# Kernel tuning notes

Hardware: AMD Instinct MI355X
Metric: run time of the kernel (lower is better)

The kernel has to match this reference:

```python
import jax, jax.numpy as jnp
import numpy as np

NH = 16  # n_heads

def setup_inputs() -> dict:
    key = jax.random.key(0)
    ks = jax.random.split(key, 5)
    B, T, D = 2, 2048, 2048
    scale = 0.02
    return {
        "x": jax.random.normal(ks[0], (B, T, D), dtype=jnp.float32),
        "Wq": jax.random.normal(ks[1], (D, D), dtype=jnp.float32) * scale,
        "Wk": jax.random.normal(ks[2], (D, D), dtype=jnp.float32) * scale,
        "Wv": jax.random.normal(ks[3], (D, D), dtype=jnp.float32) * scale,
        "Wo": jax.random.normal(ks[4], (D, D), dtype=jnp.float32) * scale,
    }

def reference(x, Wq, Wk, Wv, Wo):
    B, T, D = x.shape
    hd = D // NH
    # torch nn.Linear(d,d,bias=False): y = x @ W.T
    q = (x @ Wq.T).reshape(B, T, NH, hd).transpose(0, 2, 1, 3)  # [B,H,T,hd]
    k = (x @ Wk.T).reshape(B, T, NH, hd).transpose(0, 2, 1, 3)
    v = (x @ Wv.T).reshape(B, T, NH, hd).transpose(0, 2, 1, 3)
    att = jnp.einsum('bhtd,bhsd->bhts', q, k) / jnp.sqrt(jnp.asarray(hd, x.dtype))
    neg = jnp.finfo(att.dtype).min
    mask = jnp.triu(jnp.full((T, T), neg, dtype=att.dtype), k=1)  # causal
    att = att + mask
    w = jax.nn.softmax(att, axis=-1)
    z = jnp.einsum('bhts,bhsd->bhtd', w, v)  # [B,H,T,hd]
    z = z.transpose(0, 2, 1, 3).reshape(B, T, D)
    return z @ Wo.T
```

## Files before the change

kernel.cpp:

```cpp
#include <hip/hip_runtime.h>
#include <hip/hip_bf16.h>
#include <math.h>


typedef __attribute__((ext_vector_type(4))) float  f32x4;
typedef __attribute__((ext_vector_type(8))) __bf16 bf16x8;

union Pack8 { __bf16 h[8]; uint4 u; };
union Pack4 { __bf16 h[4]; uint2 u; };

__device__ __forceinline__ void async16(const void* g, void* l) {
    __builtin_amdgcn_global_load_lds((const __attribute__((address_space(1))) void*)g,
                                     (__attribute__((address_space(3))) void*)l, 16, 0, 0);
}

struct CvtArgs { const float* s[5]; __bf16* d[5]; };

__global__ __launch_bounds__(256) void cvt_all(CvtArgs a) {
    int i = blockIdx.x * 256 + threadIdx.x;
    int t, off;
    if (i < (1 << 20)) { t = 0; off = i; }
    else { int j = i - (1 << 20); t = 1 + (j >> 19); off = j & ((1 << 19) - 1); }
    const float4* s = (const float4*)a.s[t] + (size_t)off * 2;
    float4 f0 = s[0], f1 = s[1];
    Pack8 pk;
    pk.h[0] = (__bf16)f0.x; pk.h[1] = (__bf16)f0.y;
    pk.h[2] = (__bf16)f0.z; pk.h[3] = (__bf16)f0.w;
    pk.h[4] = (__bf16)f1.x; pk.h[5] = (__bf16)f1.y;
    pk.h[6] = (__bf16)f1.z; pk.h[7] = (__bf16)f1.w;
    ((uint4*)a.d[t])[off] = pk.u;
}

__global__ __launch_bounds__(256) void gemm_qkv(const __bf16* __restrict__ A,
        const __bf16* __restrict__ Wq, const __bf16* __restrict__ Wk,
        const __bf16* __restrict__ Wv,
        __bf16* __restrict__ Qo, __bf16* __restrict__ Ko, __bf16* __restrict__ Vt) {
    constexpr int K = 2048, N = 2048, MT = 4096;
    __shared__ __bf16 lds[32 * 512];
    __bf16* Af = lds;
    __bf16* Bf = lds + 16 * 512;
    const int tid  = threadIdx.x;
    const int w    = tid >> 6;
    const int lane = tid & 63;
    const int lm   = lane & 15;
    const int quad = lane >> 4;
    const int seg  = blockIdx.x >> 4;
    const int col0 = (blockIdx.x & 15) * 128;
    const int row0 = blockIdx.y * 128;
    const __bf16* B = (seg == 0) ? Wq : (seg == 1) ? Wk : Wv;
    const int mw = (w >> 1) * 4;
    const int nw = (w & 1) * 4;

    const __bf16* gp = (w < 2)
        ? A + (size_t)(row0 + (w * 4) * 16 + lm) * K + quad * 8
        : B + (size_t)(col0 + ((w - 2) * 4) * 16 + lm) * K + quad * 8;
    __bf16* ldst = (w < 2) ? Af + (w * 8) * 512 : Bf + ((w - 2) * 8) * 512;

    f32x4 acc[4][4] = {};

    for (int k0 = 0; k0 < K; k0 += 64) {
        __syncthreads();
#pragma unroll
        for (int i = 0; i < 8; ++i)
            async16(gp + k0 + (i >> 1) * (16 * K) + (i & 1) * 32, ldst + i * 512);
        __syncthreads();

#pragma unroll
        for (int kh = 0; kh < 2; ++kh) {
            bf16x8 af[4], bfv[4];
#pragma unroll
            for (int mt = 0; mt < 4; ++mt)
                af[mt] = *(const bf16x8*)(Af + ((mw + mt) * 2 + kh) * 512 + lane * 8);
#pragma unroll
            for (int nt = 0; nt < 4; ++nt)
                bfv[nt] = *(const bf16x8*)(Bf + ((nw + nt) * 2 + kh) * 512 + lane * 8);
#pragma unroll
            for (int mt = 0; mt < 4; ++mt)
#pragma unroll
                for (int nt = 0; nt < 4; ++nt)
                    acc[mt][nt] = __builtin_amdgcn_mfma_f32_16x16x32_bf16(
                        af[mt], bfv[nt], acc[mt][nt], 0, 0, 0);
        }
    }

    if (seg < 2) {
        __bf16* C = seg ? Ko : Qo;
#pragma unroll
        for (int mt = 0; mt < 4; ++mt)
#pragma unroll
            for (int nt = 0; nt < 4; ++nt)
#pragma unroll
                for (int r = 0; r < 4; ++r)
                    C[(size_t)(row0 + (mw + mt) * 16 + quad * 4 + r) * N +
                      col0 + (nw + nt) * 16 + lm] = (__bf16)acc[mt][nt][r];
    } else {
#pragma unroll
        for (int mt = 0; mt < 4; ++mt)
#pragma unroll
            for (int nt = 0; nt < 4; ++nt) {
                Pack4 p;
#pragma unroll
                for (int r = 0; r < 4; ++r) p.h[r] = (__bf16)acc[mt][nt][r];
                *(uint2*)&Vt[(size_t)(col0 + (nw + nt) * 16 + lm) * MT +
                             row0 + (mw + mt) * 16 + quad * 4] = p.u;
            }
    }
}

__global__ __launch_bounds__(256) void gemm_wo(const __bf16* __restrict__ A,
                                               const __bf16* __restrict__ B,
                                               float* __restrict__ C) {
    constexpr int K = 2048, N = 2048;
    __shared__ __bf16 lds[32 * 512];
    __bf16* Af = lds;
    __bf16* Bf = lds + 16 * 512;
    const int tid  = threadIdx.x;
    const int w    = tid >> 6;
    const int lane = tid & 63;
    const int lm   = lane & 15;
    const int quad = lane >> 4;
    const int row0 = blockIdx.y * 128;
    const int col0 = blockIdx.x * 128;
    const int mw   = (w >> 1) * 4;
    const int nw   = (w & 1) * 4;

    const __bf16* gp = (w < 2)
        ? A + (size_t)(row0 + (w * 4) * 16 + lm) * K + quad * 8
        : B + (size_t)(col0 + ((w - 2) * 4) * 16 + lm) * K + quad * 8;
    __bf16* ldst = (w < 2) ? Af + (w * 8) * 512 : Bf + ((w - 2) * 8) * 512;

    f32x4 acc[4][4] = {};

    for (int k0 = 0; k0 < K; k0 += 64) {
        __syncthreads();
#pragma unroll
        for (int i = 0; i < 8; ++i)
            async16(gp + k0 + (i >> 1) * (16 * K) + (i & 1) * 32, ldst + i * 512);
        __syncthreads();

#pragma unroll
        for (int kh = 0; kh < 2; ++kh) {
            bf16x8 af[4], bfv[4];
#pragma unroll
            for (int mt = 0; mt < 4; ++mt)
                af[mt] = *(const bf16x8*)(Af + ((mw + mt) * 2 + kh) * 512 + lane * 8);
#pragma unroll
            for (int nt = 0; nt < 4; ++nt)
                bfv[nt] = *(const bf16x8*)(Bf + ((nw + nt) * 2 + kh) * 512 + lane * 8);
#pragma unroll
            for (int mt = 0; mt < 4; ++mt)
#pragma unroll
                for (int nt = 0; nt < 4; ++nt)
                    acc[mt][nt] = __builtin_amdgcn_mfma_f32_16x16x32_bf16(
                        af[mt], bfv[nt], acc[mt][nt], 0, 0, 0);
        }
    }

#pragma unroll
    for (int mt = 0; mt < 4; ++mt)
#pragma unroll
        for (int nt = 0; nt < 4; ++nt)
#pragma unroll
            for (int r = 0; r < 4; ++r)
                C[(size_t)(row0 + (mw + mt) * 16 + quad * 4 + r) * N +
                  col0 + (nw + nt) * 16 + lm] = acc[mt][nt][r];
}

__global__ __launch_bounds__(256) void attn5(const __bf16* __restrict__ Q,
                                             const __bf16* __restrict__ K,
                                             const __bf16* __restrict__ Vt,
                                             __bf16* __restrict__ Z) {
    constexpr int T = 2048, D = 2048, MT = 4096, PS = 72;
    __shared__ __bf16 Kf[16 * 512];
    __shared__ __bf16 Vf[16 * 512];
    __shared__ __bf16 Pf[4 * 16 * PS];
    const int tid  = threadIdx.x;
    const int w    = tid >> 6;
    const int lane = tid & 63;
    const int lm   = lane & 15;
    const int quad = lane >> 4;
    const int f    = blockIdx.x;
    const int bh   = ((f >> 7) << 3) | (f & 7);
    const int pair = (f >> 3) & 15;
    const int b    = bh >> 4;
    const int h    = bh & 15;

    const size_t qkbase = (size_t)b * T * D + (size_t)h * 128;
    const __bf16* Qh = Q + qkbase;
    const __bf16* Kh = K + qkbase;
    const __bf16* Vh = Vt + (size_t)(h * 128) * MT + (size_t)b * T;
    __bf16* Zh = Z + qkbase;

    bf16x8 ones;
#pragma unroll
    for (int i = 0; i < 8; ++i) ones[i] = (__bf16)1.0f;

    const float c = 0.08838834764831845f;
    __bf16* pw = Pf + w * (16 * PS);

    for (int ph = 0; ph < 2; ++ph) {
        const int j  = ph ? 31 - pair : pair;
        const int q0 = j * 64 + w * 16;

        bf16x8 qf[4];
#pragma unroll
        for (int kk = 0; kk < 4; ++kk)
            qf[kk] = *(const bf16x8*)(Qh + (size_t)(q0 + lm) * D + kk * 32 + quad * 8);

        f32x4 o[8] = {};
        f32x4 osum = {};

        for (int t = 0; t <= j; ++t) {
            const int kv0 = t * 64;
            __syncthreads();
#pragma unroll
            for (int i = 0; i < 4; ++i) {
                const int fk = w * 4 + i;
                const int nt = fk >> 2, kk = fk & 3;
                async16(Kh + (size_t)(kv0 + nt * 16 + lm) * D + kk * 32 + quad * 8,
                        Kf + fk * 512);
                const int on = fk >> 1, kc = fk & 1;
                async16(Vh + (size_t)(on * 16 + lm) * MT + kv0 + kc * 32 + quad * 8,
                        Vf + fk * 512);
            }
            __syncthreads();

            f32x4 s[4] = {};
#pragma unroll
            for (int nt = 0; nt < 4; ++nt)
#pragma unroll
                for (int kk = 0; kk < 4; ++kk) {
                    bf16x8 kfr = *(const bf16x8*)(Kf + (nt * 4 + kk) * 512 + lane * 8);
                    s[nt] = __builtin_amdgcn_mfma_f32_16x16x32_bf16(qf[kk], kfr, s[nt], 0, 0, 0);
                }

            const bool diag = (t == j);
#pragma unroll
            for (int nt = 0; nt < 4; ++nt)
#pragma unroll
                for (int r = 0; r < 4; ++r) {
                    float v = s[nt][r];
                    if (diag && (kv0 + nt * 16 + lm > q0 + quad * 4 + r)) v = -1e30f;
                    s[nt][r] = __expf(fmaf(v, c, -4.0f));
                }

#pragma unroll
            for (int nt = 0; nt < 4; ++nt)
#pragma unroll
                for (int r = 0; r < 4; ++r)
                    pw[(quad * 4 + r) * PS + nt * 16 + lm] = (__bf16)s[nt][r];

            bf16x8 pf[2];
#pragma unroll
            for (int kc = 0; kc < 2; ++kc)
                pf[kc] = *(const bf16x8*)(pw + lm * PS + kc * 32 + quad * 8);

#pragma unroll
            for (int kc = 0; kc < 2; ++kc) {
                osum = __builtin_amdgcn_mfma_f32_16x16x32_bf16(pf[kc], ones, osum, 0, 0, 0);
#pragma unroll
                for (int on = 0; on < 8; ++on) {
                    bf16x8 vf = *(const bf16x8*)(Vf + (on * 2 + kc) * 512 + lane * 8);
                    o[on] = __builtin_amdgcn_mfma_f32_16x16x32_bf16(pf[kc], vf, o[on], 0, 0, 0);
                }
            }
        }

        float inv[4];
#pragma unroll
        for (int r = 0; r < 4; ++r) inv[r] = 1.f / osum[r];
#pragma unroll
        for (int on = 0; on < 8; ++on)
#pragma unroll
            for (int r = 0; r < 4; ++r)
                Zh[(size_t)(q0 + quad * 4 + r) * D + on * 16 + lm] =
                    (__bf16)(o[on][r] * inv[r]);
    }
}

extern "C" void kernel_launch(void* const* d_in, const int* in_sizes, int n_in,
                              void* d_out, int out_size, void* d_ws, size_t ws_size,
                              hipStream_t stream) {
    const float* x  = (const float*)d_in[0];
    const float* Wq = (const float*)d_in[1];
    const float* Wk = (const float*)d_in[2];
    const float* Wv = (const float*)d_in[3];
    const float* Wo = (const float*)d_in[4];
    const int D = 2048, M = 4096;
    const size_t SZ_X = (size_t)M * D;
    const size_t SZ_W = (size_t)D * D;

    __bf16* xb  = (__bf16*)d_ws;
    __bf16* Wqb = xb + SZ_X;
    __bf16* Wkb = Wqb + SZ_W;
    __bf16* Wvb = Wkb + SZ_W;
    __bf16* Wob = Wvb + SZ_W;
    __bf16* Qb  = Wob + SZ_W;
    __bf16* Kb  = Qb + SZ_X;
    __bf16* Vtb = Kb + SZ_X;
    __bf16* Zb  = xb;

    CvtArgs ca;
    ca.s[0] = x;  ca.s[1] = Wq;  ca.s[2] = Wk;  ca.s[3] = Wv;  ca.s[4] = Wo;
    ca.d[0] = xb; ca.d[1] = Wqb; ca.d[2] = Wkb; ca.d[3] = Wvb; ca.d[4] = Wob;
    cvt_all<<<12288, 256, 0, stream>>>(ca);

    gemm_qkv<<<dim3(48, 32), 256, 0, stream>>>(xb, Wqb, Wkb, Wvb, Qb, Kb, Vtb);

    attn5<<<512, 256, 0, stream>>>(Qb, Kb, Vtb, Zb);

    gemm_wo<<<dim3(16, 32), 256, 0, stream>>>(Zb, Wob, (float*)d_out);
}
```

Baseline: 461.9 us.

## Double-buffer LDS tiles in QKV, Wo GEMMs and attention kernels

Adds a two-stage LDS ping-pong to both bf16 GEMMs and the attention kernel. The next K-slice or K/V tile is issued with async global-to-LDS loads before the MFMA work on the current buffer, which removes one barrier per step and aims to hide global load latency behind compute. The GEMMs now step in 32-wide k halves, and the attention kernel's K/V staging LDS doubles. That larger footprint may lower the number of blocks resident per CU.

```diff
diff --git a/kernel.cpp b/kernel.cpp
--- a/kernel.cpp
+++ b/kernel.cpp
@@ -36,9 +36,7 @@
         const __bf16* __restrict__ Wv,
         __bf16* __restrict__ Qo, __bf16* __restrict__ Ko, __bf16* __restrict__ Vt) {
     constexpr int K = 2048, N = 2048, MT = 4096;
-    __shared__ __bf16 lds[32 * 512];
-    __bf16* Af = lds;
-    __bf16* Bf = lds + 16 * 512;
+    __shared__ __bf16 lds[2][16 * 512];
     const int tid  = threadIdx.x;
     const int w    = tid >> 6;
     const int lane = tid & 63;
@@ -51,37 +49,49 @@
     const int mw = (w >> 1) * 4;
     const int nw = (w & 1) * 4;
 
-    const __bf16* gp = (w < 2)
-        ? A + (size_t)(row0 + (w * 4) * 16 + lm) * K + quad * 8
-        : B + (size_t)(col0 + ((w - 2) * 4) * 16 + lm) * K + quad * 8;
-    __bf16* ldst = (w < 2) ? Af + (w * 8) * 512 : Bf + ((w - 2) * 8) * 512;
+    const __bf16* gA0 = A + (size_t)(row0 + (2 * w) * 16 + lm) * K + quad * 8;
+    const __bf16* gA1 = A + (size_t)(row0 + (2 * w + 1) * 16 + lm) * K + quad * 8;
+    const __bf16* gB0 = B + (size_t)(col0 + (2 * w) * 16 + lm) * K + quad * 8;
+    const __bf16* gB1 = B + (size_t)(col0 + (2 * w + 1) * 16 + lm) * K + quad * 8;
 
     f32x4 acc[4][4] = {};
 
+#define QKV_ISSUE(k0, buf)                                             \
+    do {                                                               \
+        async16(gA0 + (k0), lds[buf] + (2 * w) * 512);                 \
+        async16(gA1 + (k0), lds[buf] + (2 * w + 1) * 512);             \
+        async16(gB0 + (k0), lds[buf] + (8 + 2 * w) * 512);             \
+        async16(gB1 + (k0), lds[buf] + (8 + 2 * w + 1) * 512);         \
+    } while (0)
+
+#define QKV_COMPUTE(buf)                                               \
+    do {                                                               \
+        bf16x8 af[4], bfv[4];                                          \
+        _Pragma("unroll")                                              \
+        for (int mt = 0; mt < 4; ++mt)                                 \
+            af[mt] = *(const bf16x8*)(lds[buf] + (mw + mt) * 512 + lane * 8); \
+        _Pragma("unroll")                                              \
+        for (int nt = 0; nt < 4; ++nt)                                 \
+            bfv[nt] = *(const bf16x8*)(lds[buf] + (8 + nw + nt) * 512 + lane * 8); \
+        _Pragma("unroll")                                              \
+        for (int mt = 0; mt < 4; ++mt)                                 \
+            _Pragma("unroll")                                          \
+            for (int nt = 0; nt < 4; ++nt)                             \
+                acc[mt][nt] = __builtin_amdgcn_mfma_f32_16x16x32_bf16( \
+                    af[mt], bfv[nt], acc[mt][nt], 0, 0, 0);            \
+    } while (0)
+
+    QKV_ISSUE(0, 0);
     for (int k0 = 0; k0 < K; k0 += 64) {
         __syncthreads();
-#pragma unroll
-        for (int i = 0; i < 8; ++i)
-            async16(gp + k0 + (i >> 1) * (16 * K) + (i & 1) * 32, ldst + i * 512);
-        __syncthreads();
-
-#pragma unroll
-        for (int kh = 0; kh < 2; ++kh) {
-            bf16x8 af[4], bfv[4];
-#pragma unroll
-            for (int mt = 0; mt < 4; ++mt)
-                af[mt] = *(const bf16x8*)(Af + ((mw + mt) * 2 + kh) * 512 + lane * 8);
-#pragma unroll
-            for (int nt = 0; nt < 4; ++nt)
-                bfv[nt] = *(const bf16x8*)(Bf + ((nw + nt) * 2 + kh) * 512 + lane * 8);
-#pragma unroll
-            for (int mt = 0; mt < 4; ++mt)
-#pragma unroll
-                for (int nt = 0; nt < 4; ++nt)
-                    acc[mt][nt] = __builtin_amdgcn_mfma_f32_16x16x32_bf16(
-                        af[mt], bfv[nt], acc[mt][nt], 0, 0, 0);
-        }
+        QKV_ISSUE(k0 + 32, 1);
+        QKV_COMPUTE(0);
+        __syncthreads();
+        if (k0 + 64 < K) QKV_ISSUE(k0 + 64, 0);
+        QKV_COMPUTE(1);
     }
+#undef QKV_ISSUE
+#undef QKV_COMPUTE
 
     if (seg < 2) {
         __bf16* C = seg ? Ko : Qo;
@@ -111,9 +121,7 @@
                                                const __bf16* __restrict__ B,
                                                float* __restrict__ C) {
     constexpr int K = 2048, N = 2048;
-    __shared__ __bf16 lds[32 * 512];
-    __bf16* Af = lds;
-    __bf16* Bf = lds + 16 * 512;
+    __shared__ __bf16 lds[2][16 * 512];
     const int tid  = threadIdx.x;
     const int w    = tid >> 6;
     const int lane = tid & 63;
@@ -124,37 +132,49 @@
     const int mw   = (w >> 1) * 4;
     const int nw   = (w & 1) * 4;
 
-    const __bf16* gp = (w < 2)
-        ? A + (size_t)(row0 + (w * 4) * 16 + lm) * K + quad * 8
-        : B + (size_t)(col0 + ((w - 2) * 4) * 16 + lm) * K + quad * 8;
-    __bf16* ldst = (w < 2) ? Af + (w * 8) * 512 : Bf + ((w - 2) * 8) * 512;
+    const __bf16* gA0 = A + (size_t)(row0 + (2 * w) * 16 + lm) * K + quad * 8;
+    const __bf16* gA1 = A + (size_t)(row0 + (2 * w + 1) * 16 + lm) * K + quad * 8;
+    const __bf16* gB0 = B + (size_t)(col0 + (2 * w) * 16 + lm) * K + quad * 8;
+    const __bf16* gB1 = B + (size_t)(col0 + (2 * w + 1) * 16 + lm) * K + quad * 8;
 
     f32x4 acc[4][4] = {};
 
+#define WO_ISSUE(k0, buf)                                              \
+    do {                                                               \
+        async16(gA0 + (k0), lds[buf] + (2 * w) * 512);                 \
+        async16(gA1 + (k0), lds[buf] + (2 * w + 1) * 512);             \
+        async16(gB0 + (k0), lds[buf] + (8 + 2 * w) * 512);             \
+        async16(gB1 + (k0), lds[buf] + (8 + 2 * w + 1) * 512);         \
+    } while (0)
+
+#define WO_COMPUTE(buf)                                                \
+    do {                                                               \
+        bf16x8 af[4], bfv[4];                                          \
+        _Pragma("unroll")                                              \
+        for (int mt = 0; mt < 4; ++mt)                                 \
+            af[mt] = *(const bf16x8*)(lds[buf] + (mw + mt) * 512 + lane * 8); \
+        _Pragma("unroll")                                              \
+        for (int nt = 0; nt < 4; ++nt)                                 \
+            bfv[nt] = *(const bf16x8*)(lds[buf] + (8 + nw + nt) * 512 + lane * 8); \
+        _Pragma("unroll")                                              \
+        for (int mt = 0; mt < 4; ++mt)                                 \
+            _Pragma("unroll")                                          \
+            for (int nt = 0; nt < 4; ++nt)                             \
+                acc[mt][nt] = __builtin_amdgcn_mfma_f32_16x16x32_bf16( \
+                    af[mt], bfv[nt], acc[mt][nt], 0, 0, 0);            \
+    } while (0)
+
+    WO_ISSUE(0, 0);
     for (int k0 = 0; k0 < K; k0 += 64) {
         __syncthreads();
-#pragma unroll
-        for (int i = 0; i < 8; ++i)
-            async16(gp + k0 + (i >> 1) * (16 * K) + (i & 1) * 32, ldst + i * 512);
-        __syncthreads();
-
-#pragma unroll
-        for (int kh = 0; kh < 2; ++kh) {
-            bf16x8 af[4], bfv[4];
-#pragma unroll
-            for (int mt = 0; mt < 4; ++mt)
-                af[mt] = *(const bf16x8*)(Af + ((mw + mt) * 2 + kh) * 512 + lane * 8);
-#pragma unroll
-            for (int nt = 0; nt < 4; ++nt)
-                bfv[nt] = *(const bf16x8*)(Bf + ((nw + nt) * 2 + kh) * 512 + lane * 8);
-#pragma unroll
-            for (int mt = 0; mt < 4; ++mt)
-#pragma unroll
-                for (int nt = 0; nt < 4; ++nt)
-                    acc[mt][nt] = __builtin_amdgcn_mfma_f32_16x16x32_bf16(
-                        af[mt], bfv[nt], acc[mt][nt], 0, 0, 0);
-        }
+        WO_ISSUE(k0 + 32, 1);
+        WO_COMPUTE(0);
+        __syncthreads();
+        if (k0 + 64 < K) WO_ISSUE(k0 + 64, 0);
+        WO_COMPUTE(1);
     }
+#undef WO_ISSUE
+#undef WO_COMPUTE
 
 #pragma unroll
     for (int mt = 0; mt < 4; ++mt)
@@ -166,13 +186,12 @@
                   col0 + (nw + nt) * 16 + lm] = acc[mt][nt][r];
 }
 
-__global__ __launch_bounds__(256) void attn5(const __bf16* __restrict__ Q,
+__global__ __launch_bounds__(256) void attn6(const __bf16* __restrict__ Q,
                                              const __bf16* __restrict__ K,
                                              const __bf16* __restrict__ Vt,
                                              __bf16* __restrict__ Z) {
     constexpr int T = 2048, D = 2048, MT = 4096, PS = 72;
-    __shared__ __bf16 Kf[16 * 512];
-    __shared__ __bf16 Vf[16 * 512];
+    __shared__ __bf16 KVf[2][32 * 512];
     __shared__ __bf16 Pf[4 * 16 * PS];
     const int tid  = threadIdx.x;
     const int w    = tid >> 6;
@@ -198,6 +217,20 @@
     const float c = 0.08838834764831845f;
     __bf16* pw = Pf + w * (16 * PS);
 
+#define ATTN_ISSUE(kv0, buf)                                                     \
+    do {                                                                         \
+        _Pragma("unroll")                                                        \
+        for (int i = 0; i < 4; ++i) {                                            \
+            const int fk = w * 4 + i;                                            \
+            const int nt = fk >> 2, kk = fk & 3;                                 \
+            async16(Kh + (size_t)((kv0) + nt * 16 + lm) * D + kk * 32 + quad * 8,\
+                    KVf[buf] + fk * 512);                                        \
+            const int on = fk >> 1, kc = fk & 1;                                 \
+            async16(Vh + (size_t)(on * 16 + lm) * MT + (kv0) + kc * 32 + quad * 8,\
+                    KVf[buf] + (16 + fk) * 512);                                 \
+        }                                                                        \
+    } while (0)
+
     for (int ph = 0; ph < 2; ++ph) {
         const int j  = ph ? 31 - pair : pair;
         const int q0 = j * 64 + w * 16;
@@ -210,27 +243,24 @@
         f32x4 o[8] = {};
         f32x4 osum = {};
 
+        __syncthreads();
+        ATTN_ISSUE(0, 0);
+        int buf = 0;
+
         for (int t = 0; t <= j; ++t) {
+            __syncthreads();
+            if (t < j) ATTN_ISSUE((t + 1) * 64, buf ^ 1);
+            const __bf16* Kc = KVf[buf];
+            const __bf16* Vc = KVf[buf] + 16 * 512;
+            buf ^= 1;
             const int kv0 = t * 64;
-            __syncthreads();
-#pragma unroll
-            for (int i = 0; i < 4; ++i) {
-                const int fk = w * 4 + i;
-                const int nt = fk >> 2, kk = fk & 3;
-                async16(Kh + (size_t)(kv0 + nt * 16 + lm) * D + kk * 32 + quad * 8,
-                        Kf + fk * 512);
-                const int on = fk >> 1, kc = fk & 1;
-                async16(Vh + (size_t)(on * 16 + lm) * MT + kv0 + kc * 32 + quad * 8,
-                        Vf + fk * 512);
-            }
-            __syncthreads();
 
             f32x4 s[4] = {};
 #pragma unroll
             for (int nt = 0; nt < 4; ++nt)
 #pragma unroll
                 for (int kk = 0; kk < 4; ++kk) {
-                    bf16x8 kfr = *(const bf16x8*)(Kf + (nt * 4 + kk) * 512 + lane * 8);
+                    bf16x8 kfr = *(const bf16x8*)(Kc + (nt * 4 + kk) * 512 + lane * 8);
                     s[nt] = __builtin_amdgcn_mfma_f32_16x16x32_bf16(qf[kk], kfr, s[nt], 0, 0, 0);
                 }
 
@@ -260,7 +290,7 @@
                 osum = __builtin_amdgcn_mfma_f32_16x16x32_bf16(pf[kc], ones, osum, 0, 0, 0);
 #pragma unroll
                 for (int on = 0; on < 8; ++on) {
-                    bf16x8 vf = *(const bf16x8*)(Vf + (on * 2 + kc) * 512 + lane * 8);
+                    bf16x8 vf = *(const bf16x8*)(Vc + (on * 2 + kc) * 512 + lane * 8);
                     o[on] = __builtin_amdgcn_mfma_f32_16x16x32_bf16(pf[kc], vf, o[on], 0, 0, 0);
                 }
             }
@@ -276,6 +306,7 @@
                 Zh[(size_t)(q0 + quad * 4 + r) * D + on * 16 + lm] =
                     (__bf16)(o[on][r] * inv[r]);
     }
+#undef ATTN_ISSUE
 }
 
 extern "C" void kernel_launch(void* const* d_in, const int* in_sizes, int n_in,
@@ -307,7 +338,7 @@
 
     gemm_qkv<<<dim3(48, 32), 256, 0, stream>>>(xb, Wqb, Wkb, Wvb, Qb, Kb, Vtb);
 
-    attn5<<<512, 256, 0, stream>>>(Qb, Kb, Vtb, Zb);
+    attn6<<<512, 256, 0, stream>>>(Qb, Kb, Vtb, Zb);
 
     gemm_wo<<<dim3(16, 32), 256, 0, stream>>>(Zb, Wob, (float*)d_out);
 }
```

Measured after the change: 461.7 us. No clear change (-0.0%).
